# Optimization experiments

Hardware: AMD Instinct MI355X
Metric: run time of the kernel (lower is better)

Reference implementation:

```python
import jax, jax.numpy as jnp
import numpy as np

V = 30522
D = 768
K_DELTA = 768
BOTTLENECK = 512
B = 256
M = 4096
TEMP = 0.05
LAMBDA_REC = 1.0
LAMBDA_SPARSE = 1e-4
EPS = 1e-6


def setup_inputs() -> dict:
    key = jax.random.key(0)
    ks = jax.random.split(key, 10)
    s = lambda fan_in: 1.0 / np.sqrt(fan_in)
    return {
        "ht": jax.random.normal(ks[0], (B, V), jnp.float32),
        "sr": jax.random.uniform(ks[1], (B, V), jnp.float32),
        "z_pos": jax.random.normal(ks[2], (B, D), jnp.float32),
        "z_neg": jax.random.normal(ks[3], (M, D), jnp.float32),
        "zr": jax.random.normal(ks[4], (B, D), jnp.float32),
        "W1p": jax.random.normal(ks[5], (V, BOTTLENECK), jnp.float32) * s(V),
        "b1p": jnp.zeros((BOTTLENECK,), jnp.float32),
        "W2p": jax.random.normal(ks[6], (BOTTLENECK, V), jnp.float32) * s(BOTTLENECK),
        "b2p": jnp.zeros((V,), jnp.float32),
        "W1m": jax.random.normal(ks[7], (V, BOTTLENECK), jnp.float32) * s(V),
        "b1m": jnp.zeros((BOTTLENECK,), jnp.float32),
        "W2m": jax.random.normal(ks[8], (BOTTLENECK, V), jnp.float32) * s(BOTTLENECK),
        "b2m": jnp.zeros((V,), jnp.float32),
        "Wdec": jax.random.normal(ks[9], (V, D), jnp.float32) * s(V),
    }


def safe_l2norm(x, eps=EPS):
    return x / (jnp.linalg.norm(x, axis=-1, keepdims=True) + eps)


def _delta_branch(ht, W1, b1, W2, b2):
    # bottleneck MLP -> softplus -> topk -> scatter sparsify
    h = jax.nn.gelu(ht @ W1 + b1, approximate=False)  # torch nn.GELU default = exact erf
    u = jax.nn.softplus(h @ W2 + b2)                  # [B, V]
    vals, idx = jax.lax.top_k(u, K_DELTA)             # [B, K]
    rows = jnp.arange(u.shape[0])[:, None]
    return jnp.zeros_like(u).at[rows, idx].set(vals)  # sparse delta [B, V]


def reference(ht, sr, z_pos, z_neg, zr, W1p, b1p, W2p, b2p, W1m, b1m, W2m, b2m, Wdec):
    dsp = _delta_branch(ht, W1p, b1p, W2p, b2p)
    dsm = _delta_branch(ht, W1m, b1m, W2m, b2m)
    sqp = jnp.clip(sr + dsp, 0.0, None)
    sqm = jnp.clip(dsm, 0.0, None)
    sq = sqp - sqm
    zq = safe_l2norm(sq @ Wdec)        # DenseDecoder: Linear(V->D, bias=False) + l2norm
    zq = safe_l2norm(zq)               # re-normalized in forward_train
    z_pos_n = safe_l2norm(z_pos)
    z_neg_n = safe_l2norm(z_neg)

    pos_score = jnp.sum(zq * z_pos_n, axis=-1, keepdims=True)   # [B, 1]
    neg_score = zq @ z_neg_n.T                                   # [B, M]
    logits = jnp.concatenate([pos_score, neg_score], axis=1) / TEMP
    # cross entropy with label 0 for every row
    loss_retr = jnp.mean(jax.nn.logsumexp(logits, axis=-1) - logits[:, 0])

    zhat_r = safe_l2norm(sr @ Wdec)
    zr_n = safe_l2norm(zr)
    loss_rec = jnp.mean((zhat_r - zr_n) ** 2)

    loss_sparse = jnp.mean(jnp.sum(jnp.abs(dsp), axis=-1)) + jnp.mean(jnp.sum(jnp.abs(dsm), axis=-1))

    loss = loss_retr + LAMBDA_REC * loss_rec + LAMBDA_SPARSE * loss_sparse
    return loss
```

## Files before the change

### kernel.cpp

```cpp
#include <hip/hip_runtime.h>
#include <math.h>

#define VSZ   30522
#define DIM   768
#define KDELT 768
#define BOT   512
#define BATCH 256
#define MNEG  4096
#define EPSN  1e-6f
#define TEMPC 0.05f
#define INVT  20.0f
#define TKT   1024

typedef _Float16 f16;
typedef _Float16 f16x8 __attribute__((ext_vector_type(8)));
typedef _Float16 f16x2 __attribute__((ext_vector_type(2)));
typedef float    f32x4 __attribute__((ext_vector_type(4)));

static __device__ __forceinline__ float gelu_exact(float x){
    return 0.5f * x * (1.0f + erff(x * 0.70710678118654752440f));
}
static __device__ __forceinline__ float softplus_f(float x){
    return fmaxf(x, 0.0f) + log1pf(expf(-fabsf(x)));
}
static __device__ __forceinline__ f16x2 pkh(float a, float b){
    return __builtin_bit_cast(f16x2, __builtin_amdgcn_cvt_pkrtz(a, b));
}

template<int BSRC, int NG, int EPI, int LDA, int LDB, int N, int K, int NSPLIT>
__global__ __launch_bounds__(256, 3) void gemm32t(
    const float* __restrict__ A0, const float* __restrict__ A1,
    const float* __restrict__ B0, const float* __restrict__ B1,
    float* __restrict__ C0, float* __restrict__ C1,
    const float* __restrict__ bias0, const float* __restrict__ bias1)
{
    constexpr int MN = BATCH * N;
    __shared__ f16 Al[128][40];
    __shared__ f16 Bl[128][40];
    const int t  = threadIdx.x;
    const int m0 = blockIdx.x * 128;
    const int n0 = blockIdx.y * 128;
    const int br = blockIdx.z / NSPLIT;
    const int s  = blockIdx.z % NSPLIT;
    const float* __restrict__ A = br ? A1 : A0;
    const float* __restrict__ B = br ? B1 : B0;
    float* __restrict__ C       = br ? C1 : C0;
    const float* __restrict__ bias = br ? bias1 : bias0;

    constexpr int kchunk = ((K + NSPLIT * 32 - 1) / (NSPLIT * 32)) * 32;
    const int kb = s * kchunk;
    const int ke = min(K, kb + kchunk);

    const int ar4 = t >> 2;
    const int kq  = (t & 3) * 8;
    const int bn  = t & 127;
    const int bk2 = (t >> 7) * 16;

    const int lane = t & 63, w = t >> 6;
    const int wr = (w >> 1) * 64, wc = (w & 1) * 64;
    const int fr = lane & 15, kg = (lane >> 4) * 8;

    f32x4 acc[4][4] = {};

    float4 ra[2][2];
    float  rb[16];
    float4 rb2[2][2];

    union U8 { f16x8 v; f16x2 h[4]; };

    auto loadA = [&](int k0c, int krem) {
        #pragma unroll
        for (int p = 0; p < 2; p++) {
            const float* ap = A + (size_t)(m0 + p * 64 + ar4) * LDA + k0c + kq;
            if (krem == 32) {
                ra[p][0] = *(const float4*)ap;
                ra[p][1] = *(const float4*)(ap + 4);
            } else {
                float tm[8];
                #pragma unroll
                for (int i = 0; i < 8; i++) tm[i] = (kq + i < krem) ? ap[i] : 0.f;
                ra[p][0] = make_float4(tm[0], tm[1], tm[2], tm[3]);
                ra[p][1] = make_float4(tm[4], tm[5], tm[6], tm[7]);
            }
        }
    };
    auto loadB = [&](int k0c, int krem) {
        if (BSRC == 0) {
            const bool nok = (!NG) || (n0 + bn < N);
            if (krem == 32) {
                #pragma unroll
                for (int p = 0; p < 16; p++)
                    rb[p] = nok ? B[(size_t)(k0c + bk2 + p) * LDB + n0 + bn] : 0.f;
            } else {
                #pragma unroll
                for (int p = 0; p < 16; p++) {
                    const int kk = bk2 + p;
                    rb[p] = (kk < krem && nok) ? B[(size_t)(k0c + kk) * LDB + n0 + bn] : 0.f;
                }
            }
        } else {
            #pragma unroll
            for (int p = 0; p < 2; p++) {
                const float* bp = B + (size_t)(n0 + p * 64 + ar4) * LDB + k0c + kq;
                if (krem == 32) {
                    rb2[p][0] = *(const float4*)bp;
                    rb2[p][1] = *(const float4*)(bp + 4);
                } else {
                    float tm[8];
                    #pragma unroll
                    for (int i = 0; i < 8; i++) tm[i] = (kq + i < krem) ? bp[i] : 0.f;
                    rb2[p][0] = make_float4(tm[0], tm[1], tm[2], tm[3]);
                    rb2[p][1] = make_float4(tm[4], tm[5], tm[6], tm[7]);
                }
            }
        }
    };
    auto storeA = [&]() {
        #pragma unroll
        for (int p = 0; p < 2; p++) {
            U8 u;
            u.h[0] = pkh(ra[p][0].x, ra[p][0].y);
            u.h[1] = pkh(ra[p][0].z, ra[p][0].w);
            u.h[2] = pkh(ra[p][1].x, ra[p][1].y);
            u.h[3] = pkh(ra[p][1].z, ra[p][1].w);
            *(f16x8*)&Al[p * 64 + ar4][kq] = u.v;
        }
    };
    auto storeB = [&]() {
        if (BSRC == 0) {
            U8 u0, u1;
            u0.h[0] = pkh(rb[0],  rb[1]);
            u0.h[1] = pkh(rb[2],  rb[3]);
            u0.h[2] = pkh(rb[4],  rb[5]);
            u0.h[3] = pkh(rb[6],  rb[7]);
            u1.h[0] = pkh(rb[8],  rb[9]);
            u1.h[1] = pkh(rb[10], rb[11]);
            u1.h[2] = pkh(rb[12], rb[13]);
            u1.h[3] = pkh(rb[14], rb[15]);
            *(f16x8*)&Bl[bn][bk2]     = u0.v;
            *(f16x8*)&Bl[bn][bk2 + 8] = u1.v;
        } else {
            #pragma unroll
            for (int p = 0; p < 2; p++) {
                U8 u;
                u.h[0] = pkh(rb2[p][0].x, rb2[p][0].y);
                u.h[1] = pkh(rb2[p][0].z, rb2[p][0].w);
                u.h[2] = pkh(rb2[p][1].x, rb2[p][1].y);
                u.h[3] = pkh(rb2[p][1].z, rb2[p][1].w);
                *(f16x8*)&Bl[p * 64 + ar4][kq] = u.v;
            }
        }
    };

    int k0 = kb;
    {
        const int kr = min(32, ke - k0);
        loadA(k0, kr); loadB(k0, kr);
    }
    while (k0 < ke) {
        storeA(); storeB();
        __syncthreads();
        const int k1 = k0 + 32;
        if (k1 < ke) {
            const int kr = min(32, ke - k1);
            loadA(k1, kr); loadB(k1, kr);
        }
        f16x8 af[4], bf[4];
        #pragma unroll
        for (int m = 0; m < 4; m++) af[m] = *(const f16x8*)&Al[wr + m * 16 + fr][kg];
        #pragma unroll
        for (int n = 0; n < 4; n++) bf[n] = *(const f16x8*)&Bl[wc + n * 16 + fr][kg];
        #pragma unroll
        for (int m = 0; m < 4; m++)
            #pragma unroll
            for (int n = 0; n < 4; n++)
                acc[m][n] = __builtin_amdgcn_mfma_f32_16x16x32_f16(af[m], bf[n], acc[m][n], 0, 0, 0);
        __syncthreads();
        k0 = k1;
    }

    float* Cp = (EPI == 0) ? (C + (size_t)s * MN) : C;
    #pragma unroll
    for (int m = 0; m < 4; m++) {
        #pragma unroll
        for (int n = 0; n < 4; n++) {
            #pragma unroll
            for (int j = 0; j < 4; j++) {
                const int row = m0 + wr + m * 16 + (lane >> 4) * 4 + j;
                const int col = n0 + wc + n * 16 + fr;
                if (NG && col >= N) continue;
                if (EPI == 0) Cp[(size_t)row * N + col] = acc[m][n][j];
                else          Cp[(size_t)row * N + col] = softplus_f(acc[m][n][j] + bias[col]);
            }
        }
    }
}

__global__ __launch_bounds__(256) void reduce_bias_gelu2(
    const float* __restrict__ P0, const float* __restrict__ P1,
    const float* __restrict__ bias0, const float* __restrict__ bias1,
    float* __restrict__ H0, float* __restrict__ H1,
    int MN, int N, int nsplit)
{
    const int idx = blockIdx.x * 256 + threadIdx.x;
    if (idx >= MN) return;
    const int n = idx % N;
    const float* P = blockIdx.y ? P1 : P0;
    const float* bias = blockIdx.y ? bias1 : bias0;
    float* H = blockIdx.y ? H1 : H0;
    float s = 0.f;
    for (int k = 0; k < nsplit; k++) s += P[(size_t)k * MN + idx];
    H[idx] = gelu_exact(s + bias[n]);
}

__global__ __launch_bounds__(256) void reduce_sum_parts(
    const float* __restrict__ P, float* __restrict__ Y, int MN, int nsplit)
{
    const int idx = blockIdx.x * 256 + threadIdx.x;
    if (idx >= MN) return;
    float s = 0.f;
    for (int k = 0; k < nsplit; k++) s += P[(size_t)k * MN + idx];
    Y[idx] = s;
}

__global__ __launch_bounds__(TKT) void topk_thresh2(
    const float* __restrict__ U1, const float* __restrict__ U2,
    float* __restrict__ tP, float* __restrict__ tM)
{
    __shared__ unsigned int hist[4096];
    __shared__ unsigned int scan[TKT];
    __shared__ unsigned int s_pref;
    __shared__ int s_rem;
    const int row = blockIdx.y, t = threadIdx.x;
    const float* u = (blockIdx.x ? U2 : U1) + (size_t)row * VSZ;
    float* tout = blockIdx.x ? tM : tP;

    unsigned int pref = 0;
    int remain = KDELT;

    #pragma unroll
    for (int p = 0; p < 3; p++) {
        for (int i = t; i < 4096; i += TKT) hist[i] = 0;
        __syncthreads();
        for (int j = t; j < VSZ / 2; j += TKT) {
            const float2 x = *(const float2*)(u + 2 * j);
            const unsigned int v0 = __float_as_uint(x.x);
            const unsigned int v1 = __float_as_uint(x.y);
            if (p == 0) {
                atomicAdd(&hist[v0 >> 19], 1u);
                atomicAdd(&hist[v1 >> 19], 1u);
            } else if (p == 1) {
                if ((v0 >> 19) == pref) atomicAdd(&hist[(v0 >> 7) & 0xFFFu], 1u);
                if ((v1 >> 19) == pref) atomicAdd(&hist[(v1 >> 7) & 0xFFFu], 1u);
            } else {
                if ((v0 >> 7) == pref) atomicAdd(&hist[v0 & 0x7Fu], 1u);
                if ((v1 >> 7) == pref) atomicAdd(&hist[v1 & 0x7Fu], 1u);
            }
        }
        __syncthreads();
        unsigned int loc = hist[4 * t] + hist[4 * t + 1] + hist[4 * t + 2] + hist[4 * t + 3];
        scan[t] = loc;
        __syncthreads();
        for (int o = 1; o < TKT; o <<= 1) {
            const unsigned int v = (t + o < TKT) ? scan[t + o] : 0u;
            __syncthreads();
            scan[t] += v;
            __syncthreads();
        }
        const unsigned int above = (t + 1 < TKT) ? scan[t + 1] : 0u;
        if (scan[t] >= (unsigned int)remain && above < (unsigned int)remain) {
            unsigned int cum = above;
            #pragma unroll
            for (int bi = 3; bi >= 0; bi--) {
                const int b = 4 * t + bi;
                cum += hist[b];
                if (cum >= (unsigned int)remain) {
                    s_pref = (unsigned int)b;
                    s_rem  = remain - (int)(cum - hist[b]);
                    break;
                }
            }
        }
        __syncthreads();
        if (p == 0)      pref = s_pref;
        else if (p == 1) pref = (pref << 12) | s_pref;
        else             pref = (pref << 7)  | s_pref;
        remain = s_rem;
        __syncthreads();
    }
    if (t == 0) tout[row] = __uint_as_float(pref);
}

__global__ __launch_bounds__(256) void build_sq(
    float* __restrict__ U1, const float* __restrict__ U2,
    const float* __restrict__ sr,
    const float* __restrict__ tp, const float* __restrict__ tm,
    float* __restrict__ sparse_p, float* __restrict__ sparse_m)
{
    __shared__ float red[256];
    const int row = blockIdx.x, t = threadIdx.x;
    const float thp = tp[row], thm = tm[row];
    float* u1 = U1 + (size_t)row * VSZ;
    const float* u2 = U2 + (size_t)row * VSZ;
    const float* s  = sr + (size_t)row * VSZ;
    float sp = 0.f, sm = 0.f;
    for (int j = t; j < VSZ / 2; j += 256) {
        const float2 up = *(const float2*)(u1 + 2 * j);
        const float2 um = *(const float2*)(u2 + 2 * j);
        const float2 ss = *(const float2*)(s  + 2 * j);
        const float dp0 = (up.x >= thp) ? up.x : 0.f;
        const float dp1 = (up.y >= thp) ? up.y : 0.f;
        const float dm0 = (um.x >= thm) ? um.x : 0.f;
        const float dm1 = (um.y >= thm) ? um.y : 0.f;
        sp += dp0 + dp1; sm += dm0 + dm1;
        float2 o;
        o.x = fmaxf(ss.x + dp0, 0.f) - fmaxf(dm0, 0.f);
        o.y = fmaxf(ss.y + dp1, 0.f) - fmaxf(dm1, 0.f);
        *(float2*)(u1 + 2 * j) = o;
    }
    red[t] = sp; __syncthreads();
    for (int o = 128; o > 0; o >>= 1) { if (t < o) red[t] += red[t + o]; __syncthreads(); }
    if (t == 0) sparse_p[row] = red[0];
    __syncthreads();
    red[t] = sm; __syncthreads();
    for (int o = 128; o > 0; o >>= 1) { if (t < o) red[t] += red[t + o]; __syncthreads(); }
    if (t == 0) sparse_m[row] = red[0];
}

__global__ __launch_bounds__(256) void rownorm(
    const float* __restrict__ X, float* __restrict__ Y, int dbl)
{
    __shared__ float red[256];
    const int row = blockIdx.x, t = threadIdx.x;
    const float* x = X + (size_t)row * DIM;
    float* y = Y + (size_t)row * DIM;
    float v0 = x[t], v1 = x[t + 256], v2 = x[t + 512];
    red[t] = v0 * v0 + v1 * v1 + v2 * v2; __syncthreads();
    for (int o = 128; o > 0; o >>= 1) { if (t < o) red[t] += red[t + o]; __syncthreads(); }
    const float nrm = sqrtf(red[0]) + EPSN;
    v0 /= nrm; v1 /= nrm; v2 /= nrm;
    if (dbl) {
        __syncthreads();
        red[t] = v0 * v0 + v1 * v1 + v2 * v2; __syncthreads();
        for (int o = 128; o > 0; o >>= 1) { if (t < o) red[t] += red[t + o]; __syncthreads(); }
        const float n2 = sqrtf(red[0]) + EPSN;
        v0 /= n2; v1 /= n2; v2 /= n2;
    }
    y[t] = v0; y[t + 256] = v1; y[t + 512] = v2;
}

__global__ __launch_bounds__(256) void pos_dot(
    const float* __restrict__ zq, const float* __restrict__ zp,
    float* __restrict__ posL)
{
    __shared__ float red[256];
    const int row = blockIdx.x, t = threadIdx.x;
    const float* a = zq + (size_t)row * DIM;
    const float* b = zp + (size_t)row * DIM;
    red[t] = a[t] * b[t] + a[t + 256] * b[t + 256] + a[t + 512] * b[t + 512];
    __syncthreads();
    for (int o = 128; o > 0; o >>= 1) { if (t < o) red[t] += red[t + o]; __syncthreads(); }
    if (t == 0) posL[row] = red[0] / TEMPC;
}

__global__ __launch_bounds__(256) void lse_loss(
    const float* __restrict__ negL, const float* __restrict__ posL,
    float* __restrict__ rowL)
{
    __shared__ float red[256];
    const int row = blockIdx.x, t = threadIdx.x;
    const float* nl = negL + (size_t)row * MNEG;
    const float p = posL[row];
    float lmax = (t == 0) ? p : -INFINITY;
    for (int j = t; j < MNEG; j += 256) lmax = fmaxf(lmax, nl[j] * INVT);
    red[t] = lmax; __syncthreads();
    for (int o = 128; o > 0; o >>= 1) { if (t < o) red[t] = fmaxf(red[t], red[t + o]); __syncthreads(); }
    const float mx = red[0];
    __syncthreads();
    float lsum = (t == 0) ? expf(p - mx) : 0.f;
    for (int j = t; j < MNEG; j += 256) lsum += expf(nl[j] * INVT - mx);
    red[t] = lsum; __syncthreads();
    for (int o = 128; o > 0; o >>= 1) { if (t < o) red[t] += red[t + o]; __syncthreads(); }
    if (t == 0) rowL[row] = mx + logf(red[0]) - p;
}

__global__ __launch_bounds__(256) void rec_row(
    const float* __restrict__ zhat, const float* __restrict__ zrn,
    float* __restrict__ part)
{
    __shared__ float red[256];
    const int row = blockIdx.x, t = threadIdx.x;
    const float* a = zhat + (size_t)row * DIM;
    const float* b = zrn + (size_t)row * DIM;
    const float d0 = a[t] - b[t], d1 = a[t + 256] - b[t + 256], d2 = a[t + 512] - b[t + 512];
    red[t] = d0 * d0 + d1 * d1 + d2 * d2;
    __syncthreads();
    for (int o = 128; o > 0; o >>= 1) { if (t < o) red[t] += red[t + o]; __syncthreads(); }
    if (t == 0) part[row] = red[0];
}

__global__ __launch_bounds__(256) void final_combine(
    const float* __restrict__ rowL, const float* __restrict__ recP,
    const float* __restrict__ spP, const float* __restrict__ spM,
    float* __restrict__ out)
{
    __shared__ float red[256];
    const int t = threadIdx.x;
    red[t] = rowL[t]; __syncthreads();
    for (int o = 128; o > 0; o >>= 1) { if (t < o) red[t] += red[t + o]; __syncthreads(); }
    const float retr = red[0] / 256.0f;
    __syncthreads();
    red[t] = recP[t]; __syncthreads();
    for (int o = 128; o > 0; o >>= 1) { if (t < o) red[t] += red[t + o]; __syncthreads(); }
    const float rec = red[0] / (float)(BATCH * DIM);
    __syncthreads();
    red[t] = spP[t] + spM[t]; __syncthreads();
    for (int o = 128; o > 0; o >>= 1) { if (t < o) red[t] += red[t + o]; __syncthreads(); }
    const float sparse = red[0] / 256.0f;
    if (t == 0) out[0] = retr + 1.0f * rec + 1e-4f * sparse;
}

extern "C" void kernel_launch(void* const* d_in, const int* in_sizes, int n_in,
                              void* d_out, int out_size, void* d_ws, size_t ws_size,
                              hipStream_t stream)
{
    const float* ht   = (const float*)d_in[0];
    const float* sr   = (const float*)d_in[1];
    const float* zpos = (const float*)d_in[2];
    const float* zneg = (const float*)d_in[3];
    const float* zr   = (const float*)d_in[4];
    const float* W1p  = (const float*)d_in[5];
    const float* b1p  = (const float*)d_in[6];
    const float* W2p  = (const float*)d_in[7];
    const float* b2p  = (const float*)d_in[8];
    const float* W1m  = (const float*)d_in[9];
    const float* b1m  = (const float*)d_in[10];
    const float* W2m  = (const float*)d_in[11];
    const float* b2m  = (const float*)d_in[12];
    const float* Wdec = (const float*)d_in[13];
    float* out = (float*)d_out;

    char* ws = (char*)d_ws;
    float* U1   = (float*)(ws + 0);
    float* U2   = (float*)(ws + 31254528);
    float* P    = (float*)(ws + 62509056);
    float* Hp   = (float*)(ws + 96063488);
    float* Hm   = (float*)(ws + 96587776);
    float* Y1   = (float*)(ws + 97112064);
    float* Y2   = (float*)(ws + 97898496);
    float* Zn   = (float*)(ws + 98684928);
    float* Zp   = (float*)(ws + 111267840);
    float* Zrn  = (float*)(ws + 112054272);
    float* NegL = (float*)(ws + 112840704);
    float* tP   = (float*)(ws + 117035008);
    float* tM   = tP + 256;
    float* spP  = tP + 512;
    float* spM  = tP + 768;
    float* posL = tP + 1024;
    float* rowL = tP + 1280;
    float* recP = tP + 1536;
    (void)in_sizes; (void)n_in; (void)out_size; (void)ws_size;

    const dim3 blk(256);

    gemm32t<0,0,0, VSZ, BOT, BOT, VSZ, 56><<<dim3(2,4,112), blk, 0, stream>>>(
        ht, ht, W1p, W1m, U1, U2, nullptr, nullptr);
    reduce_bias_gelu2<<<dim3(512,2), blk, 0, stream>>>(
        U1, U2, b1p, b1m, Hp, Hm, BATCH*BOT, BOT, 56);

    gemm32t<0,1,1, BOT, VSZ, VSZ, BOT, 1><<<dim3(2,239,2), blk, 0, stream>>>(
        Hp, Hm, W2p, W2m, U1, U2, b2p, b2m);

    topk_thresh2<<<dim3(2,256), dim3(TKT), 0, stream>>>(U1, U2, tP, tM);
    build_sq<<<dim3(256), blk, 0, stream>>>(U1, U2, sr, tP, tM, spP, spM);

    gemm32t<0,0,0, VSZ, DIM, DIM, VSZ, 32><<<dim3(2,6,64), blk, 0, stream>>>(
        U1, sr, Wdec, Wdec, P, U2, nullptr, nullptr);
    reduce_sum_parts<<<dim3(768), blk, 0, stream>>>(P,  Y1, BATCH*DIM, 32);
    reduce_sum_parts<<<dim3(768), blk, 0, stream>>>(U2, Y2, BATCH*DIM, 32);

    rownorm<<<dim3(256),  blk, 0, stream>>>(Y1, Y1, 1);
    rownorm<<<dim3(256),  blk, 0, stream>>>(Y2, Y2, 0);
    rownorm<<<dim3(4096), blk, 0, stream>>>(zneg, Zn, 0);
    rownorm<<<dim3(256),  blk, 0, stream>>>(zpos, Zp, 0);
    rownorm<<<dim3(256),  blk, 0, stream>>>(zr,   Zrn, 0);

    pos_dot<<<dim3(256), blk, 0, stream>>>(Y1, Zp, posL);
    gemm32t<1,0,0, DIM, DIM, MNEG, DIM, 8><<<dim3(2,32,8), blk, 0, stream>>>(
        Y1, Y1, Zn, Zn, P, P, nullptr, nullptr);
    reduce_sum_parts<<<dim3(4096), blk, 0, stream>>>(P, NegL, BATCH*MNEG, 8);
    lse_loss<<<dim3(256), blk, 0, stream>>>(NegL, posL, rowL);

    rec_row<<<dim3(256), blk, 0, stream>>>(Y2, Zrn, recP);

    final_combine<<<dim3(1), blk, 0, stream>>>(rowL, recP, spP, spM, out);
}
```

Before: 466.6 us.

## Defer softplus past top-k, retune split-K counts and launch bounds

Since softplus is monotonic, the second-layer GEMM now writes raw pre-activations, and the top-k radix select runs on order-preserving float keys so it handles negative values. Softplus is applied only to the selected entries in build_sq, which avoids evaluating a transcendental for every vocabulary element. The first GEMM's split-K count drops from 56 to 32 and now writes partials to a separate buffer region, the negatives GEMM split drops from 8 to 4, and launch bounds go from 3 to 2 blocks per CU. The split and occupancy changes trade partial-sum traffic and register pressure against parallelism.

```diff
diff --git a/kernel.cpp b/kernel.cpp
--- a/kernel.cpp
+++ b/kernel.cpp
@@ -26,9 +26,13 @@
 static __device__ __forceinline__ f16x2 pkh(float a, float b){
     return __builtin_bit_cast(f16x2, __builtin_amdgcn_cvt_pkrtz(a, b));
 }
+static __device__ __forceinline__ unsigned int fkey(float f){
+    const unsigned int u = __float_as_uint(f);
+    return u ^ (((unsigned int)((int)u >> 31)) | 0x80000000u);
+}
 
 template<int BSRC, int NG, int EPI, int LDA, int LDB, int N, int K, int NSPLIT>
-__global__ __launch_bounds__(256, 3) void gemm32t(
+__global__ __launch_bounds__(256, 2) void gemm32t(
     const float* __restrict__ A0, const float* __restrict__ A1,
     const float* __restrict__ B0, const float* __restrict__ B1,
     float* __restrict__ C0, float* __restrict__ C1,
@@ -190,7 +194,7 @@
                 const int col = n0 + wc + n * 16 + fr;
                 if (NG && col >= N) continue;
                 if (EPI == 0) Cp[(size_t)row * N + col] = acc[m][n][j];
-                else          Cp[(size_t)row * N + col] = softplus_f(acc[m][n][j] + bias[col]);
+                else          Cp[(size_t)row * N + col] = acc[m][n][j] + bias[col];
             }
         }
     }
@@ -244,17 +248,17 @@
         __syncthreads();
         for (int j = t; j < VSZ / 2; j += TKT) {
             const float2 x = *(const float2*)(u + 2 * j);
-            const unsigned int v0 = __float_as_uint(x.x);
-            const unsigned int v1 = __float_as_uint(x.y);
+            const unsigned int k0 = fkey(x.x);
+            const unsigned int k1 = fkey(x.y);
             if (p == 0) {
-                atomicAdd(&hist[v0 >> 19], 1u);
-                atomicAdd(&hist[v1 >> 19], 1u);
+                atomicAdd(&hist[k0 >> 20], 1u);
+                atomicAdd(&hist[k1 >> 20], 1u);
             } else if (p == 1) {
-                if ((v0 >> 19) == pref) atomicAdd(&hist[(v0 >> 7) & 0xFFFu], 1u);
-                if ((v1 >> 19) == pref) atomicAdd(&hist[(v1 >> 7) & 0xFFFu], 1u);
+                if ((k0 >> 20) == pref) atomicAdd(&hist[(k0 >> 8) & 0xFFFu], 1u);
+                if ((k1 >> 20) == pref) atomicAdd(&hist[(k1 >> 8) & 0xFFFu], 1u);
             } else {
-                if ((v0 >> 7) == pref) atomicAdd(&hist[v0 & 0x7Fu], 1u);
-                if ((v1 >> 7) == pref) atomicAdd(&hist[v1 & 0x7Fu], 1u);
+                if ((k0 >> 8) == pref) atomicAdd(&hist[k0 & 0xFFu], 1u);
+                if ((k1 >> 8) == pref) atomicAdd(&hist[k1 & 0xFFu], 1u);
             }
         }
         __syncthreads();
@@ -284,11 +288,14 @@
         __syncthreads();
         if (p == 0)      pref = s_pref;
         else if (p == 1) pref = (pref << 12) | s_pref;
-        else             pref = (pref << 7)  | s_pref;
+        else             pref = (pref << 8)  | s_pref;
         remain = s_rem;
         __syncthreads();
     }
-    if (t == 0) tout[row] = __uint_as_float(pref);
+    if (t == 0) {
+        const unsigned int u2 = (pref & 0x80000000u) ? (pref ^ 0x80000000u) : ~pref;
+        tout[row] = __uint_as_float(u2);
+    }
 }
 
 __global__ __launch_bounds__(256) void build_sq(
@@ -308,14 +315,14 @@
         const float2 up = *(const float2*)(u1 + 2 * j);
         const float2 um = *(const float2*)(u2 + 2 * j);
         const float2 ss = *(const float2*)(s  + 2 * j);
-        const float dp0 = (up.x >= thp) ? up.x : 0.f;
-        const float dp1 = (up.y >= thp) ? up.y : 0.f;
-        const float dm0 = (um.x >= thm) ? um.x : 0.f;
-        const float dm1 = (um.y >= thm) ? um.y : 0.f;
+        const float dp0 = (up.x >= thp) ? softplus_f(up.x) : 0.f;
+        const float dp1 = (up.y >= thp) ? softplus_f(up.y) : 0.f;
+        const float dm0 = (um.x >= thm) ? softplus_f(um.x) : 0.f;
+        const float dm1 = (um.y >= thm) ? softplus_f(um.y) : 0.f;
         sp += dp0 + dp1; sm += dm0 + dm1;
         float2 o;
-        o.x = fmaxf(ss.x + dp0, 0.f) - fmaxf(dm0, 0.f);
-        o.y = fmaxf(ss.y + dp1, 0.f) - fmaxf(dm1, 0.f);
+        o.x = fmaxf(ss.x + dp0, 0.f) - dm0;
+        o.y = fmaxf(ss.y + dp1, 0.f) - dm1;
         *(float2*)(u1 + 2 * j) = o;
     }
     red[t] = sp; __syncthreads();
@@ -444,6 +451,7 @@
     float* U1   = (float*)(ws + 0);
     float* U2   = (float*)(ws + 31254528);
     float* P    = (float*)(ws + 62509056);
+    float* P1g  = (float*)(ws + 62509056 + 16777216);
     float* Hp   = (float*)(ws + 96063488);
     float* Hm   = (float*)(ws + 96587776);
     float* Y1   = (float*)(ws + 97112064);
@@ -463,10 +471,10 @@
 
     const dim3 blk(256);
 
-    gemm32t<0,0,0, VSZ, BOT, BOT, VSZ, 56><<<dim3(2,4,112), blk, 0, stream>>>(
-        ht, ht, W1p, W1m, U1, U2, nullptr, nullptr);
+    gemm32t<0,0,0, VSZ, BOT, BOT, VSZ, 32><<<dim3(2,4,64), blk, 0, stream>>>(
+        ht, ht, W1p, W1m, P, P1g, nullptr, nullptr);
     reduce_bias_gelu2<<<dim3(512,2), blk, 0, stream>>>(
-        U1, U2, b1p, b1m, Hp, Hm, BATCH*BOT, BOT, 56);
+        P, P1g, b1p, b1m, Hp, Hm, BATCH*BOT, BOT, 32);
 
     gemm32t<0,1,1, BOT, VSZ, VSZ, BOT, 1><<<dim3(2,239,2), blk, 0, stream>>>(
         Hp, Hm, W2p, W2m, U1, U2, b2p, b2m);
@@ -486,9 +494,9 @@
     rownorm<<<dim3(256),  blk, 0, stream>>>(zr,   Zrn, 0);
 
     pos_dot<<<dim3(256), blk, 0, stream>>>(Y1, Zp, posL);
-    gemm32t<1,0,0, DIM, DIM, MNEG, DIM, 8><<<dim3(2,32,8), blk, 0, stream>>>(
+    gemm32t<1,0,0, DIM, DIM, MNEG, DIM, 4><<<dim3(2,32,4), blk, 0, stream>>>(
         Y1, Y1, Zn, Zn, P, P, nullptr, nullptr);
-    reduce_sum_parts<<<dim3(4096), blk, 0, stream>>>(P, NegL, BATCH*MNEG, 8);
+    reduce_sum_parts<<<dim3(4096), blk, 0, stream>>>(P, NegL, BATCH*MNEG, 4);
     lse_loss<<<dim3(256), blk, 0, stream>>>(NegL, posL, rowL);
 
     rec_row<<<dim3(256), blk, 0, stream>>>(Y2, Zrn, recP);
```

Result: faster. 437.6 us (-6.2%).
